# Optimization experiments

Measured on AMD Instinct MI355X. Metric: run time of the kernel, lower is better.

Reference implementation:

```python
import jax, jax.numpy as jnp
import numpy as np

SPATIAL, CROP = 128, 256


def definePsf(N, M, slope):
    # standard LCT psf (O'Toole et al.), as used in Wenzheng Chen's torch port
    x = (np.arange(2 * N, dtype=np.float32) / (2 * N - 1)) * 2 - 1
    z = (np.arange(2 * M, dtype=np.float32) / (2 * M - 1)) * 2
    gy, gx = np.meshgrid(x, x)
    psf = np.abs(((4 * slope) ** 2) * (gx[None] ** 2 + gy[None] ** 2) - z[:, None, None])
    psf = (psf == psf.min(axis=0, keepdims=True)).astype(np.float32)
    psf = psf / psf[:, N, N].sum()
    psf = psf / np.linalg.norm(psf.ravel())
    psf = np.roll(psf, N, axis=1)
    psf = np.roll(psf, N, axis=2)
    return psf


def resamplingOperator(M):
    row = M ** 2
    x = np.arange(row, dtype=np.float64) + 1
    mtx = np.zeros((row, M), dtype=np.float64)
    mtx[np.arange(row), (np.ceil(np.sqrt(x)) - 1).astype(np.int64)] = 1
    mtx = mtx / x[:, None]
    mtxi = mtx.T.copy()
    for _ in range(int(np.log2(M))):
        mtx = 0.5 * (mtx[0::2] + mtx[1::2])
        mtxi = 0.5 * (mtxi[:, 0::2] + mtxi[:, 1::2])
    return mtx.astype(np.float32), mtxi.astype(np.float32)


def setup_inputs() -> dict:
    key = jax.random.key(0)
    k1, k2 = jax.random.split(key)
    B, D, T, H = 1, 1, CROP, SPATIAL
    feture = jax.random.uniform(k1, (B, D, T, H, H), dtype=jnp.float32)

    c = 3e8
    bin_len = 0.01
    wall_size = 2.0
    trange = CROP * c * (bin_len / c)
    slope = (wall_size / 2.0) / trange
    psf = definePsf(SPATIAL, CROP, slope)
    fpsf = np.fft.fftn(psf)
    snr = 0.1
    invpsf = np.conjugate(fpsf) / (1.0 / snr + np.real(fpsf) ** 2 + np.imag(fpsf) ** 2)

    mtx, mtxi = resamplingOperator(CROP)
    gridz = (np.arange(CROP, dtype=np.float32) / (CROP - 1)).reshape(1, CROP, 1, 1)
    learnable_w = 0.01 * jax.random.normal(k2, (2,) + psf.shape, dtype=jnp.float32)

    return dict(
        feture=feture,
        gridz=jnp.asarray(gridz),
        mtx=jnp.asarray(mtx),
        mtxi=jnp.asarray(mtxi),
        invpsf_real=jnp.asarray(np.real(invpsf).astype(np.float32)),
        invpsf_imag=jnp.asarray(np.imag(invpsf).astype(np.float32)),
        learnable_w=learnable_w,
    )


def reference(feture, gridz, mtx, mtxi, invpsf_real, invpsf_imag, learnable_w):
    B, D, T, H, W = feture.shape
    # diffuse falloff compensation: * z^4
    data = feture.reshape(B * D, T, H, W) * gridz ** 4
    # temporal resampling GEMM: [M,T] @ [BD,T,HW]
    tmp = jnp.einsum('mt,bthw->bmhw', mtx, data)
    # zero-pad to 2T x 2H x 2W
    pad = jnp.zeros((B * D, 2 * T, 2 * H, 2 * W), jnp.float32).at[:, :T, :H, :W].set(tmp)
    # full (non-onesided) complex 3D FFT of real data
    fre = jnp.fft.fftn(pad, axes=(1, 2, 3))
    # learned + fixed inverse filter in frequency domain
    wf = (learnable_w[0] + invpsf_real) + 1j * (learnable_w[1] + invpsf_imag)
    vol = jnp.fft.ifftn(fre * wf, axes=(1, 2, 3)).real[:, :T, :H, :W]
    # inverse temporal resampling GEMM
    out = jnp.einsum('mt,bthw->bmhw', mtxi, vol)
    return out.reshape(B, D, T, H, W)
```

## Files before the change

kernel.cpp:

```cpp
#include <hip/hip_runtime.h>
#include <math.h>

#define TC 256
#define HC 128
#define Z2 512
#define Y2 256
#define X2 256
#define HW 16384
#define LSTR256 260
#define LSTR512 519
#define MTSH 4
#define MT (1<<MTSH)
#define WPAD 132
#define KZS 257

__device__ __forceinline__ float2 cadd(float2 a, float2 b){ return make_float2(a.x+b.x, a.y+b.y); }
__device__ __forceinline__ float2 csub(float2 a, float2 b){ return make_float2(a.x-b.x, a.y-b.y); }

template<int SGN>
__device__ __forceinline__ float2 cmul_tw(float2 z, float2 w){
  float wy = (SGN < 0) ? w.y : -w.y;
  return make_float2(z.x*w.x - z.y*wy, z.x*wy + z.y*w.x);
}
template<int SGN>
__device__ __forceinline__ float2 mul_pmi(float2 t){
  return (SGN < 0) ? make_float2(t.y, -t.x) : make_float2(-t.y, t.x);
}

template<int SGN>
__device__ __forceinline__ void dft16(float2 r[16], const float2* __restrict__ tw){
  float2 u[16];
  #pragma unroll
  for (int b2=0;b2<4;b2++){
    float2 x0=r[b2], x1=r[4+b2], x2=r[8+b2], x3=r[12+b2];
    float2 t0=cadd(x0,x2), t1=csub(x0,x2), t2=cadd(x1,x3), t3=csub(x1,x3);
    float2 y0=cadd(t0,t2), y2=csub(t0,t2);
    float2 t3i = mul_pmi<SGN>(t3);
    float2 y1=cadd(t1,t3i), y3=csub(t1,t3i);
    u[0*4+b2]=y0;
    u[1*4+b2]=cmul_tw<SGN>(y1, tw[(16*b2)&255]);
    u[2*4+b2]=cmul_tw<SGN>(y2, tw[(32*b2)&255]);
    u[3*4+b2]=cmul_tw<SGN>(y3, tw[(48*b2)&255]);
  }
  #pragma unroll
  for (int e2=0;e2<4;e2++){
    float2 x0=u[e2*4+0], x1=u[e2*4+1], x2=u[e2*4+2], x3=u[e2*4+3];
    float2 t0=cadd(x0,x2), t1=csub(x0,x2), t2=cadd(x1,x3), t3=csub(x1,x3);
    float2 t3i = mul_pmi<SGN>(t3);
    r[0*4+e2]=cadd(t0,t2);
    r[1*4+e2]=cadd(t1,t3i);
    r[2*4+e2]=csub(t0,t2);
    r[3*4+e2]=csub(t1,t3i);
  }
}

template<int SGN>
__device__ __forceinline__ void fft256(float2* ln, int b, const float2* __restrict__ tw){
  float2 r[16];
  #pragma unroll
  for (int a=0;a<16;a++) r[a] = ln[16*a+b];
  dft16<SGN>(r, tw);
  #pragma unroll
  for (int e=1;e<16;e++) r[e] = cmul_tw<SGN>(r[e], tw[(b*e)&255]);
  __syncthreads();
  #pragma unroll
  for (int e=0;e<16;e++) ln[16*e+b] = r[e];
  __syncthreads();
  #pragma unroll
  for (int a=0;a<16;a++) r[a] = ln[16*b+a];
  dft16<SGN>(r, tw);
  __syncthreads();
  #pragma unroll
  for (int d=0;d<16;d++) ln[16*d+b] = r[d];
  __syncthreads();
}

template<int SGN, bool CROP_OUT>
__device__ __forceinline__ void fft512(float2* ln, int lt,
        const float2* __restrict__ tw256, const float2* __restrict__ tw512){
  int team = lt >> 4, b = lt & 15;
  float2* sc = ln + team*256;
  float2 r[16];
  #pragma unroll
  for (int a=0;a<16;a++) r[a] = ln[2*(16*a+b) + team];
  dft16<SGN>(r, tw256);
  #pragma unroll
  for (int e=1;e<16;e++) r[e] = cmul_tw<SGN>(r[e], tw256[(b*e)&255]);
  __syncthreads();
  #pragma unroll
  for (int e=0;e<16;e++) sc[16*e+b] = r[e];
  __syncthreads();
  #pragma unroll
  for (int a=0;a<16;a++) r[a] = sc[16*b+a];
  dft16<SGN>(r, tw256);
  __syncthreads();
  if (team==0){
    #pragma unroll
    for (int d=0;d<16;d++) ln[16*d+b] = r[d];
  } else {
    #pragma unroll
    for (int d=0;d<16;d++){ int k=16*d+b; ln[256+k] = cmul_tw<SGN>(r[d], tw512[k]); }
  }
  __syncthreads();
  float2 res[8], res2[8];
  #pragma unroll
  for (int j=0;j<8;j++){
    int k = lt + 32*j;
    float2 E = ln[k], WO = ln[256+k];
    res[j]  = cadd(E,WO);
    res2[j] = csub(E,WO);
  }
  __syncthreads();
  #pragma unroll
  for (int j=0;j<8;j++){
    int k = lt + 32*j;
    ln[k] = res[j];
    if (!CROP_OUT) ln[256+k] = res2[j];
  }
  __syncthreads();
}

__global__ void k_init_tw(float2* tw256, float2* tw512){
  int j = threadIdx.x;
  if (j < 512){
    double a = -6.283185307179586476925286766559 * (double)j / 512.0;
    tw512[j] = make_float2((float)cos(a), (float)sin(a));
  }
  if (j < 256){
    double a = -6.283185307179586476925286766559 * (double)j / 256.0;
    tw256[j] = make_float2((float)cos(a), (float)sin(a));
  }
}

__global__ __launch_bounds__(256) void k_gemm(const float* __restrict__ A,
    const float* __restrict__ Bv, const float* __restrict__ gz, float* __restrict__ C){
  __shared__ float As[64][MT];
  __shared__ float zz[256];
  int tid = threadIdx.x;
  int hw0 = blockIdx.x*512 + tid*2;
  int m0 = blockIdx.y*MT;
  float2 acc[MT];
  #pragma unroll
  for (int i=0;i<MT;i++) acc[i]=make_float2(0.f,0.f);
  {
    float s = 1.f;
    if (gz){ float g = gz[tid]; float g2=g*g; s = g2*g2; }
    zz[tid] = s;
  }
  for (int t0=0;t0<256;t0+=64){
    __syncthreads();
    #pragma unroll
    for (int e=0;e<(64*MT)/256;e++){
      int idx = e*256 + tid;
      int tt = idx >> MTSH, mi = idx & (MT-1);
      As[tt][mi] = A[(size_t)(m0+mi)*256 + t0 + tt] * zz[t0+tt];
    }
    __syncthreads();
    for (int ts=0;ts<64;ts+=8){
      float2 v[8];
      #pragma unroll
      for (int j=0;j<8;j++) v[j] = *(const float2*)(Bv + (size_t)(t0+ts+j)*HW + hw0);
      #pragma unroll
      for (int j=0;j<8;j++){
        const float4* row = (const float4*)&As[ts+j][0];
        #pragma unroll
        for (int q=0;q<MT/4;q++){
          float4 a4 = row[q];
          acc[4*q+0].x += a4.x*v[j].x; acc[4*q+0].y += a4.x*v[j].y;
          acc[4*q+1].x += a4.y*v[j].x; acc[4*q+1].y += a4.y*v[j].y;
          acc[4*q+2].x += a4.z*v[j].x; acc[4*q+2].y += a4.z*v[j].y;
          acc[4*q+3].x += a4.w*v[j].x; acc[4*q+3].y += a4.w*v[j].y;
        }
      }
    }
  }
  #pragma unroll
  for (int mi=0;mi<MT;mi++) *(float2*)(C + (size_t)(m0+mi)*HW + hw0) = acc[mi];
}

__global__ __launch_bounds__(512) void k_fft_zf(const float* __restrict__ tmp,
      float2* __restrict__ A, const float2* __restrict__ tw256, const float2* __restrict__ tw512){
  __shared__ float2 buf[16*LSTR512];
  int tid = threadIdx.x;
  int hwl = tid & 15, ng = tid >> 4;
  int hw = blockIdx.x*16 + hwl;
  size_t colbase = (size_t)(hw>>7)*WPAD + (hw & 127);
  float2* ln = buf + hwl*LSTR512;
  #pragma unroll
  for (int a=0;a<8;a++){
    int n = a*32 + ng;
    ln[n] = make_float2(tmp[(size_t)n*HW + hw], 0.f);
  }
  #pragma unroll
  for (int a=8;a<16;a++){
    int n = a*32 + ng;
    ln[n] = make_float2(0.f,0.f);
  }
  __syncthreads();
  fft512<-1,false>(ln, ng, tw256, tw512);
  #pragma unroll
  for (int a=0;a<8;a++){
    int n = a*32 + ng;
    A[(size_t)n*(128*WPAD) + colbase] = ln[n];
  }
  if (ng==0) A[(size_t)256*(128*WPAD) + colbase] = ln[256];
}

__global__ __launch_bounds__(256) void k_fft_yf(const float2* __restrict__ A,
      float2* __restrict__ B, const float2* __restrict__ tw256){
  __shared__ float2 buf[16*LSTR256];
  int tid = threadIdx.x;
  int w = tid & 15, b = tid >> 4;
  int kz = blockIdx.x;
  int wx = blockIdx.y*16 + w;
  float2* ln = buf + w*LSTR256;
  size_t abase = (size_t)kz*(128*WPAD) + wx;
  #pragma unroll
  for (int a=0;a<8;a++){
    int n = 16*a + b;
    ln[n] = A[abase + (size_t)n*WPAD];
    ln[n+128] = make_float2(0.f,0.f);
  }
  __syncthreads();
  fft256<-1>(ln, b, tw256);
  size_t bbase = (size_t)kz*(256*WPAD) + wx;
  #pragma unroll
  for (int a=0;a<16;a++){
    int n = 16*a + b;
    B[bbase + (size_t)n*WPAD] = ln[n];
  }
}

__global__ __launch_bounds__(256) void k_x_filt(float2* __restrict__ B,
      const float* __restrict__ R, const float* __restrict__ I,
      const float* __restrict__ w0, const float* __restrict__ w1,
      const float2* __restrict__ tw256){
  __shared__ float2 buf[16*LSTR256];
  const float sc = 1.f/33554432.f;
  int tid = threadIdx.x;
  int wl = tid >> 4, b = tid & 15;
  int kz = blockIdx.y;
  int ky = blockIdx.x*16 + wl;
  float2* ln = buf + wl*LSTR256;
  size_t rb = ((size_t)kz*256 + ky)*WPAD;
  #pragma unroll
  for (int a=0;a<8;a++){
    int n = 16*a + b;
    ln[n] = B[rb + n];
    ln[n+128] = make_float2(0.f,0.f);
  }
  __syncthreads();
  fft256<-1>(ln, b, tw256);
  unsigned mz = (512u - (unsigned)kz) & 511u;
  unsigned my = (256u - (unsigned)ky) & 255u;
  size_t trow = ((size_t)kz<<16) + (size_t)ky*256;
  size_t mrow = ((size_t)mz<<16) + (size_t)my*256;
  const float* Rrow  = R  + trow;
  const float* Irow  = I  + trow;
  const float* w0row = w0 + trow;
  const float* w1row = w1 + trow;
  const float* w0mr  = w0 + mrow;
  const float* w1mr  = w1 + mrow;
  #pragma unroll
  for (int L=0; L<4; ++L){
    int k0 = L*64 + 4*b;
    float4 Rf  = *(const float4*)(Rrow  + k0);
    float4 If  = *(const float4*)(Irow  + k0);
    float4 w0f = *(const float4*)(w0row + k0);
    float4 w1f = *(const float4*)(w1row + k0);
    float4 q0 = *(const float4*)(w0mr + 252 - k0);
    float4 q1 = *(const float4*)(w1mr + 252 - k0);
    float s0 = w0mr[(256 - k0) & 255];
    float s1 = w1mr[(256 - k0) & 255];
    float w0m0=s0, w0m1=q0.w, w0m2=q0.z, w0m3=q0.y;
    float w1m0=s1, w1m1=q1.w, w1m2=q1.z, w1m3=q1.y;
    float wr0=(Rf.x+0.5f*(w0f.x+w0m0))*sc, wi0=(If.x+0.5f*(w1f.x-w1m0))*sc;
    float wr1=(Rf.y+0.5f*(w0f.y+w0m1))*sc, wi1=(If.y+0.5f*(w1f.y-w1m1))*sc;
    float wr2=(Rf.z+0.5f*(w0f.z+w0m2))*sc, wi2=(If.z+0.5f*(w1f.z-w1m2))*sc;
    float wr3=(Rf.w+0.5f*(w0f.w+w0m3))*sc, wi3=(If.w+0.5f*(w1f.w-w1m3))*sc;
    float2 v0=ln[k0], v1=ln[k0+1], v2=ln[k0+2], v3=ln[k0+3];
    ln[k0]   = make_float2(v0.x*wr0 - v0.y*wi0, v0.x*wi0 + v0.y*wr0);
    ln[k0+1] = make_float2(v1.x*wr1 - v1.y*wi1, v1.x*wi1 + v1.y*wr1);
    ln[k0+2] = make_float2(v2.x*wr2 - v2.y*wi2, v2.x*wi2 + v2.y*wr2);
    ln[k0+3] = make_float2(v3.x*wr3 - v3.y*wi3, v3.x*wi3 + v3.y*wr3);
  }
  __syncthreads();
  fft256<1>(ln, b, tw256);
  #pragma unroll
  for (int a=0;a<8;a++){
    int n = 16*a + b;
    B[rb + n] = ln[n];
  }
}

__global__ __launch_bounds__(256) void k_fft_yi(const float2* __restrict__ B,
      float2* __restrict__ A, const float2* __restrict__ tw256){
  __shared__ float2 buf[16*LSTR256];
  int tid = threadIdx.x;
  int w = tid & 15, b = tid >> 4;
  int kz = blockIdx.x;
  int wx = blockIdx.y*16 + w;
  float2* ln = buf + w*LSTR256;
  size_t bbase = (size_t)kz*(256*WPAD) + wx;
  #pragma unroll
  for (int a=0;a<16;a++){
    int n = 16*a + b;
    ln[n] = B[bbase + (size_t)n*WPAD];
  }
  __syncthreads();
  fft256<1>(ln, b, tw256);
  size_t abase = (size_t)kz*(128*WPAD) + wx;
  #pragma unroll
  for (int a=0;a<8;a++){
    int n = 16*a + b;
    A[abase + (size_t)n*WPAD] = ln[n];
  }
}

__global__ __launch_bounds__(512) void k_fft_zi(const float2* __restrict__ A,
      float* __restrict__ vol, const float2* __restrict__ tw256, const float2* __restrict__ tw512){
  __shared__ float2 buf[16*LSTR512];
  int tid = threadIdx.x;
  int hwl = tid & 15, ng = tid >> 4;
  int hw = blockIdx.x*16 + hwl;
  size_t colbase = (size_t)(hw>>7)*WPAD + (hw & 127);
  float2* ln = buf + hwl*LSTR512;
  #pragma unroll
  for (int a=0;a<8;a++){
    int n = a*32 + ng;
    ln[n] = A[(size_t)n*(128*WPAD) + colbase];
  }
  if (ng==0) ln[256] = A[(size_t)256*(128*WPAD) + colbase];
  __syncthreads();
  #pragma unroll
  for (int a=8;a<16;a++){
    int n = a*32 + ng;
    if (n > 256){ float2 v = ln[512-n]; ln[n] = make_float2(v.x, -v.y); }
  }
  __syncthreads();
  fft512<1,true>(ln, ng, tw256, tw512);
  #pragma unroll
  for (int a=0;a<8;a++){
    int n = a*32 + ng;
    vol[(size_t)n*HW + hw] = ln[n].x;
  }
}

extern "C" void kernel_launch(void* const* d_in, const int* in_sizes, int n_in,
                              void* d_out, int out_size, void* d_ws, size_t ws_size,
                              hipStream_t stream) {
  const float* fet = (const float*)d_in[0];
  const float* gz  = (const float*)d_in[1];
  const float* mtx = (const float*)d_in[2];
  const float* mtxi= (const float*)d_in[3];
  const float* Rr  = (const float*)d_in[4];
  const float* Ii  = (const float*)d_in[5];
  const float* lw  = (const float*)d_in[6];
  const float* w0  = lw;
  const float* w1  = lw + (size_t)Z2*Y2*X2;
  float* out = (float*)d_out;

  char* ws = (char*)d_ws;
  const size_t OFF_TW256 = 0;
  const size_t OFF_TW512 = 2048;
  const size_t OFF_TMP   = 8192;
  const size_t TMP_BYTES = (size_t)TC*HW*sizeof(float);
  const size_t OFF_A     = OFF_TMP + TMP_BYTES;
  const size_t A_BYTES   = (size_t)KZS*128*WPAD*sizeof(float2);
  const size_t OFF_B     = OFF_A + A_BYTES;
  const size_t B_BYTES   = (size_t)KZS*256*WPAD*sizeof(float2);
  const size_t NEED      = OFF_B + B_BYTES;
  if (ws_size < NEED) return;

  float2* tw256 = (float2*)(ws + OFF_TW256);
  float2* tw512 = (float2*)(ws + OFF_TW512);
  float*  tmp   = (float*)(ws + OFF_TMP);
  float*  vol   = (float*)(ws + OFF_TMP);
  float2* A     = (float2*)(ws + OFF_A);
  float2* B     = (float2*)(ws + OFF_B);

  hipLaunchKernelGGL(k_init_tw, dim3(1), dim3(512), 0, stream, tw256, tw512);
  hipLaunchKernelGGL(k_gemm, dim3(32,256/MT), dim3(256), 0, stream, mtx, fet, gz, tmp);
  hipLaunchKernelGGL(k_fft_zf, dim3(1024), dim3(512), 0, stream, tmp, A, tw256, tw512);
  hipLaunchKernelGGL(k_fft_yf, dim3(KZS,8), dim3(256), 0, stream, A, B, tw256);
  hipLaunchKernelGGL(k_x_filt, dim3(16,KZS), dim3(256), 0, stream, B, Rr, Ii, w0, w1, tw256);
  hipLaunchKernelGGL(k_fft_yi, dim3(KZS,8), dim3(256), 0, stream, B, A, tw256);
  hipLaunchKernelGGL(k_fft_zi, dim3(1024), dim3(512), 0, stream, A, vol, tw256, tw512);
  hipLaunchKernelGGL(k_gemm, dim3(32,256/MT), dim3(256), 0, stream, mtxi, vol, (const float*)nullptr, out);
}
```

Before: 298.4 us.

## Fuse temporal resampling GEMMs into the z-axis FFT kernels

Folds the forward resampling GEMM (with the z^4 falloff scaling) into the forward z-FFT kernel and the inverse GEMM into the inverse z-FFT kernel. Each block computes the GEMM for its 16 spatial columns directly in shared memory. This removes the tmp/vol intermediate buffers, their global round trips, and two launches. In exchange, every block re-streams the full 256x256 matrix from L2/global, reads input rows in small 64-byte chunks, and the inverse kernel uses more shared memory, which may lower occupancy.

Measured after the change: 407.2 us. +36.5%, slower.

```diff
diff --git a/kernel.cpp b/kernel.cpp
--- a/kernel.cpp
+++ b/kernel.cpp
@@ -9,10 +9,9 @@
 #define HW 16384
 #define LSTR256 260
 #define LSTR512 519
-#define MTSH 4
-#define MT (1<<MTSH)
 #define WPAD 132
 #define KZS 257
+#define MPAD 36
 
 __device__ __forceinline__ float2 cadd(float2 a, float2 b){ return make_float2(a.x+b.x, a.y+b.y); }
 __device__ __forceinline__ float2 csub(float2 a, float2 b){ return make_float2(a.x-b.x, a.y-b.y); }
@@ -132,71 +131,65 @@
   }
 }
 
-__global__ __launch_bounds__(256) void k_gemm(const float* __restrict__ A,
-    const float* __restrict__ Bv, const float* __restrict__ gz, float* __restrict__ C){
-  __shared__ float As[64][MT];
-  __shared__ float zz[256];
+__global__ __launch_bounds__(512) void k_zf_gemm(const float* __restrict__ mtxg,
+      const float* __restrict__ fet, const float* __restrict__ gz,
+      float2* __restrict__ A, const float2* __restrict__ tw256, const float2* __restrict__ tw512){
+  __shared__ float2 buf[16*LSTR512];
+  float* S = (float*)buf;
+  float* mtx_s = S;
+  float* d_s   = S + 256*MPAD;
+  float* zz    = S + 256*MPAD + 16*MPAD;
   int tid = threadIdx.x;
-  int hw0 = blockIdx.x*512 + tid*2;
-  int m0 = blockIdx.y*MT;
-  float2 acc[MT];
-  #pragma unroll
-  for (int i=0;i<MT;i++) acc[i]=make_float2(0.f,0.f);
-  {
-    float s = 1.f;
-    if (gz){ float g = gz[tid]; float g2=g*g; s = g2*g2; }
-    zz[tid] = s;
-  }
-  for (int t0=0;t0<256;t0+=64){
-    __syncthreads();
-    #pragma unroll
-    for (int e=0;e<(64*MT)/256;e++){
-      int idx = e*256 + tid;
-      int tt = idx >> MTSH, mi = idx & (MT-1);
-      As[tt][mi] = A[(size_t)(m0+mi)*256 + t0 + tt] * zz[t0+tt];
+  int hwbase = blockIdx.x*16;
+  if (tid < 256){ float g = gz[tid]; float g2 = g*g; zz[tid] = g2*g2; }
+  __syncthreads();
+  int c2 = tid & 7, g8 = tid >> 3;
+  float acc0[4] = {0.f,0.f,0.f,0.f};
+  float acc1[4] = {0.f,0.f,0.f,0.f};
+  for (int tc=0; tc<8; ++tc){
+    #pragma unroll
+    for (int e=0;e<16;e++){
+      int idx = e*512 + tid;
+      int n = idx >> 5, tl = idx & 31;
+      mtx_s[n*MPAD + tl] = mtxg[n*256 + tc*32 + tl];
+    }
+    {
+      int tl = tid >> 4, hwl = tid & 15;
+      d_s[hwl*MPAD + tl] = fet[(size_t)(tc*32+tl)*HW + hwbase + hwl] * zz[tc*32+tl];
     }
     __syncthreads();
-    for (int ts=0;ts<64;ts+=8){
-      float2 v[8];
+    float4 dr0[8], dr1[8];
+    const float4* d0 = (const float4*)(d_s + (2*c2)*MPAD);
+    const float4* d1 = (const float4*)(d_s + (2*c2+1)*MPAD);
+    #pragma unroll
+    for (int q=0;q<8;q++){ dr0[q]=d0[q]; dr1[q]=d1[q]; }
+    #pragma unroll
+    for (int a=0;a<4;a++){
+      const float4* mrow = (const float4*)(mtx_s + (a*64+g8)*MPAD);
+      float s0=0.f, s1=0.f;
       #pragma unroll
-      for (int j=0;j<8;j++) v[j] = *(const float2*)(Bv + (size_t)(t0+ts+j)*HW + hw0);
-      #pragma unroll
-      for (int j=0;j<8;j++){
-        const float4* row = (const float4*)&As[ts+j][0];
-        #pragma unroll
-        for (int q=0;q<MT/4;q++){
-          float4 a4 = row[q];
-          acc[4*q+0].x += a4.x*v[j].x; acc[4*q+0].y += a4.x*v[j].y;
-          acc[4*q+1].x += a4.y*v[j].x; acc[4*q+1].y += a4.y*v[j].y;
-          acc[4*q+2].x += a4.z*v[j].x; acc[4*q+2].y += a4.z*v[j].y;
-          acc[4*q+3].x += a4.w*v[j].x; acc[4*q+3].y += a4.w*v[j].y;
-        }
+      for (int q=0;q<8;q++){
+        float4 m = mrow[q];
+        s0 += m.x*dr0[q].x + m.y*dr0[q].y + m.z*dr0[q].z + m.w*dr0[q].w;
+        s1 += m.x*dr1[q].x + m.y*dr1[q].y + m.z*dr1[q].z + m.w*dr1[q].w;
       }
+      acc0[a]+=s0; acc1[a]+=s1;
     }
-  }
-  #pragma unroll
-  for (int mi=0;mi<MT;mi++) *(float2*)(C + (size_t)(m0+mi)*HW + hw0) = acc[mi];
-}
-
-__global__ __launch_bounds__(512) void k_fft_zf(const float* __restrict__ tmp,
-      float2* __restrict__ A, const float2* __restrict__ tw256, const float2* __restrict__ tw512){
-  __shared__ float2 buf[16*LSTR512];
-  int tid = threadIdx.x;
+    __syncthreads();
+  }
+  #pragma unroll
+  for (int a=0;a<4;a++){
+    int n = a*64 + g8;
+    buf[(2*c2)*LSTR512 + n]         = make_float2(acc0[a], 0.f);
+    buf[(2*c2+1)*LSTR512 + n]       = make_float2(acc1[a], 0.f);
+    buf[(2*c2)*LSTR512 + 256 + n]   = make_float2(0.f,0.f);
+    buf[(2*c2+1)*LSTR512 + 256 + n] = make_float2(0.f,0.f);
+  }
+  __syncthreads();
   int hwl = tid & 15, ng = tid >> 4;
-  int hw = blockIdx.x*16 + hwl;
+  int hw = hwbase + hwl;
   size_t colbase = (size_t)(hw>>7)*WPAD + (hw & 127);
   float2* ln = buf + hwl*LSTR512;
-  #pragma unroll
-  for (int a=0;a<8;a++){
-    int n = a*32 + ng;
-    ln[n] = make_float2(tmp[(size_t)n*HW + hw], 0.f);
-  }
-  #pragma unroll
-  for (int a=8;a<16;a++){
-    int n = a*32 + ng;
-    ln[n] = make_float2(0.f,0.f);
-  }
-  __syncthreads();
   fft512<-1,false>(ln, ng, tw256, tw512);
   #pragma unroll
   for (int a=0;a<8;a++){
@@ -317,12 +310,15 @@
   }
 }
 
-__global__ __launch_bounds__(512) void k_fft_zi(const float2* __restrict__ A,
-      float* __restrict__ vol, const float2* __restrict__ tw256, const float2* __restrict__ tw512){
+__global__ __launch_bounds__(512) void k_zi_gemm(const float2* __restrict__ A,
+      const float* __restrict__ mtxig, float* __restrict__ out,
+      const float2* __restrict__ tw256, const float2* __restrict__ tw512){
   __shared__ float2 buf[16*LSTR512];
+  __shared__ float mtxi_s[256*MPAD];
   int tid = threadIdx.x;
+  int hwbase = blockIdx.x*16;
   int hwl = tid & 15, ng = tid >> 4;
-  int hw = blockIdx.x*16 + hwl;
+  int hw = hwbase + hwl;
   size_t colbase = (size_t)(hw>>7)*WPAD + (hw & 127);
   float2* ln = buf + hwl*LSTR512;
   #pragma unroll
@@ -339,10 +335,37 @@
   }
   __syncthreads();
   fft512<1,true>(ln, ng, tw256, tw512);
-  #pragma unroll
-  for (int a=0;a<8;a++){
-    int n = a*32 + ng;
-    vol[(size_t)n*HW + hw] = ln[n].x;
+  int c2 = tid & 7, g8 = tid >> 3;
+  const float2* v0 = buf + (2*c2)*LSTR512;
+  const float2* v1 = buf + (2*c2+1)*LSTR512;
+  float acc0[4] = {0.f,0.f,0.f,0.f};
+  float acc1[4] = {0.f,0.f,0.f,0.f};
+  for (int tc=0; tc<8; ++tc){
+    #pragma unroll
+    for (int e=0;e<16;e++){
+      int idx = e*512 + tid;
+      int m = idx >> 5, tl = idx & 31;
+      mtxi_s[m*MPAD + tl] = mtxig[m*256 + tc*32 + tl];
+    }
+    __syncthreads();
+    #pragma unroll
+    for (int q=0;q<8;q++){
+      int t0 = tc*32 + 4*q;
+      float2 a0=v0[t0], b0=v0[t0+1], c0=v0[t0+2], d0=v0[t0+3];
+      float2 a1=v1[t0], b1=v1[t0+1], c1=v1[t0+2], d1=v1[t0+3];
+      #pragma unroll
+      for (int a=0;a<4;a++){
+        float4 m4 = *(const float4*)(mtxi_s + (a*64+g8)*MPAD + 4*q);
+        acc0[a] += m4.x*a0.x + m4.y*b0.x + m4.z*c0.x + m4.w*d0.x;
+        acc1[a] += m4.x*a1.x + m4.y*b1.x + m4.z*c1.x + m4.w*d1.x;
+      }
+    }
+    __syncthreads();
+  }
+  #pragma unroll
+  for (int a=0;a<4;a++){
+    int m = a*64 + g8;
+    *(float2*)(out + (size_t)m*HW + hwbase + 2*c2) = make_float2(acc0[a], acc1[a]);
   }
 }
 
@@ -363,9 +386,7 @@
   char* ws = (char*)d_ws;
   const size_t OFF_TW256 = 0;
   const size_t OFF_TW512 = 2048;
-  const size_t OFF_TMP   = 8192;
-  const size_t TMP_BYTES = (size_t)TC*HW*sizeof(float);
-  const size_t OFF_A     = OFF_TMP + TMP_BYTES;
+  const size_t OFF_A     = 8192;
   const size_t A_BYTES   = (size_t)KZS*128*WPAD*sizeof(float2);
   const size_t OFF_B     = OFF_A + A_BYTES;
   const size_t B_BYTES   = (size_t)KZS*256*WPAD*sizeof(float2);
@@ -374,17 +395,13 @@
 
   float2* tw256 = (float2*)(ws + OFF_TW256);
   float2* tw512 = (float2*)(ws + OFF_TW512);
-  float*  tmp   = (float*)(ws + OFF_TMP);
-  float*  vol   = (float*)(ws + OFF_TMP);
   float2* A     = (float2*)(ws + OFF_A);
   float2* B     = (float2*)(ws + OFF_B);
 
   hipLaunchKernelGGL(k_init_tw, dim3(1), dim3(512), 0, stream, tw256, tw512);
-  hipLaunchKernelGGL(k_gemm, dim3(32,256/MT), dim3(256), 0, stream, mtx, fet, gz, tmp);
-  hipLaunchKernelGGL(k_fft_zf, dim3(1024), dim3(512), 0, stream, tmp, A, tw256, tw512);
+  hipLaunchKernelGGL(k_zf_gemm, dim3(1024), dim3(512), 0, stream, mtx, fet, gz, A, tw256, tw512);
   hipLaunchKernelGGL(k_fft_yf, dim3(KZS,8), dim3(256), 0, stream, A, B, tw256);
   hipLaunchKernelGGL(k_x_filt, dim3(16,KZS), dim3(256), 0, stream, B, Rr, Ii, w0, w1, tw256);
   hipLaunchKernelGGL(k_fft_yi, dim3(KZS,8), dim3(256), 0, stream, B, A, tw256);
-  hipLaunchKernelGGL(k_fft_zi, dim3(1024), dim3(512), 0, stream, A, vol, tw256, tw512);
-  hipLaunchKernelGGL(k_gemm, dim3(32,256/MT), dim3(256), 0, stream, mtxi, vol, (const float*)nullptr, out);
-}
+  hipLaunchKernelGGL(k_zi_gemm, dim3(1024), dim3(512), 0, stream, A, mtxi, out, tw256, tw512);
+}
```
